# Performance work log

Measured on AMD Instinct MI355X. Metric: run time of the kernel, lower is better.

## Reference

```python
import jax, jax.numpy as jnp
import numpy as np
import math

HEADS = 16
D = 1024
HEAD_DIM = D // HEADS
SEQ = 2048
BATCH = 4
LN_EPS = 1e-5


def setup_inputs() -> dict:
    key = jax.random.key(0)
    ks = jax.random.split(key, 7)
    s = 1.0 / math.sqrt(HEAD_DIM)
    return {
        "q": jax.random.normal(ks[0], (SEQ, BATCH, D), dtype=jnp.float32),
        "k": jax.random.normal(ks[1], (SEQ, BATCH, D), dtype=jnp.float32),
        "v": jax.random.normal(ks[2], (SEQ, BATCH, D), dtype=jnp.float32),
        "Wq": jax.random.normal(ks[3], (HEAD_DIM, HEAD_DIM), dtype=jnp.float32) * s,
        "Wk": jax.random.normal(ks[4], (HEAD_DIM, HEAD_DIM), dtype=jnp.float32) * s,
        "Wv": jax.random.normal(ks[5], (HEAD_DIM, HEAD_DIM), dtype=jnp.float32) * s,
        "Wl": jax.random.normal(ks[6], (D, D), dtype=jnp.float32) * (1.0 / math.sqrt(D)),
        "gamma": jnp.ones((D,), dtype=jnp.float32),
        "beta": jnp.zeros((D,), dtype=jnp.float32),
    }


def reference(q, k, v, Wq, Wk, Wv, Wl, gamma, beta):
    # q, k, v: [seq_len, batch, d]  (seq-first, as in the torch module)
    q_len, batch = q.shape[0], q.shape[1]
    k_len, v_len = k.shape[0], v.shape[0]
    # Faithful to torch: reshape (NOT transpose) seq-first tensor into
    # (batch, len, heads, head_dim), then per-head linear (x @ W.T, no bias).
    Qh = jnp.einsum('bqhd,ed->bqhe', q.reshape(batch, q_len, HEADS, HEAD_DIM), Wq)
    Kh = jnp.einsum('bkhd,ed->bkhe', k.reshape(batch, k_len, HEADS, HEAD_DIM), Wk)
    Vh = jnp.einsum('bvhd,ed->bvhe', v.reshape(batch, v_len, HEADS, HEAD_DIM), Wv)
    # Scores scaled by sqrt(d) (full model dim), as in the original.
    scores = jnp.einsum('bqhd,bkhd->bhqk', Qh, Kh) / math.sqrt(D)
    attn = jax.nn.softmax(scores, axis=-1)  # dropout p=0.0 -> identity
    out = jnp.einsum('bhqk,bkhd->bqhd', attn, Vh)  # [b, q, h, d]
    concat = out.reshape(q_len, batch, D)
    lin = concat @ Wl.T
    mean = jnp.mean(lin, axis=-1, keepdims=True)
    var = jnp.var(lin, axis=-1, keepdims=True)
    ln = (lin - mean) * jax.lax.rsqrt(var + LN_EPS) * gamma + beta
    return q + ln
```

## Files before the change

kernel.cpp:

```cpp
#include <hip/hip_runtime.h>

#define LOG2E 1.4426950408889634f

typedef __attribute__((ext_vector_type(8))) short short8_t;
typedef __attribute__((ext_vector_type(4))) float floatx4;
typedef __attribute__((ext_vector_type(16))) float floatx16;

#define MFMA(a,b,c)   __builtin_amdgcn_mfma_f32_16x16x32_bf16(a,b,c,0,0,0)
#define MFMA32(a,b,c) __builtin_amdgcn_mfma_f32_32x32x16_bf16(a,b,c,0,0,0)
#define GLOAD(g, l) __builtin_amdgcn_global_load_lds( \
    (const __attribute__((address_space(1))) unsigned int*)(g), \
    (__attribute__((address_space(3))) unsigned int*)(l), 16, 0, 0)

__device__ __forceinline__ unsigned short f2bf(float f){
    unsigned u = __float_as_uint(f);
    u = u + 0x7FFFu + ((u >> 16) & 1u);
    return (unsigned short)(u >> 16);
}
__device__ __forceinline__ float bf2f(unsigned short s){
    return __uint_as_float(((unsigned)s) << 16);
}
__device__ __forceinline__ unsigned cvtpk(float lo, float hi){
    unsigned r;
    asm("v_cvt_pk_bf16_f32 %0, %1, %2" : "=v"(r) : "v"(lo), "v"(hi));
    return r;
}
__device__ __forceinline__ void plswap(unsigned &a, unsigned &b){
    asm volatile("v_permlane32_swap_b32 %0, %1" : "+v"(a), "+v"(b));
}

union U8 { unsigned u[4]; short8_t s8; };


__global__ __launch_bounds__(256) void proj_kernel(
    const float* __restrict__ Xq, const float* __restrict__ Xk, const float* __restrict__ Xv,
    const float* __restrict__ Wq, const float* __restrict__ Wk, const float* __restrict__ Wv,
    unsigned short* __restrict__ qp, unsigned short* __restrict__ kp, unsigned short* __restrict__ vp)
{
    const int rt = blockIdx.x;
    const int h  = blockIdx.y;
    const int sel= blockIdx.z;
    const float* X = (sel==0)?Xq:(sel==1)?Xk:Xv;
    const float* W = (sel==0)?Wq:(sel==1)?Wk:Wv;
    unsigned short* O = (sel==0)?qp:(sel==1)?kp:vp;
    const float qs = (sel==0) ? ((1.0f/32.0f)*LOG2E) : 1.0f;

    const int t  = threadIdx.x;
    const int w  = t >> 6, l = t & 63;
    const int r5 = l & 31;
    const int hf = l >> 5;

    const int row0 = rt*128 + w*32;

    short8_t a[4];
    {
        const float* xb = X + (size_t)(row0 + r5)*1024 + h*64 + hf*8;
        #pragma unroll
        for (int kb=0; kb<4; kb++){
            float4 f0 = *reinterpret_cast<const float4*>(xb + kb*16);
            float4 f1 = *reinterpret_cast<const float4*>(xb + kb*16 + 4);
            U8 u;
            u.u[0] = cvtpk(f0.x, f0.y); u.u[1] = cvtpk(f0.z, f0.w);
            u.u[2] = cvtpk(f1.x, f1.y); u.u[3] = cvtpk(f1.z, f1.w);
            a[kb] = u.s8;
        }
    }
    short8_t b[2][4];
    #pragma unroll
    for (int nb=0; nb<2; nb++){
        const float* wb = W + (size_t)(nb*32 + r5)*64 + hf*8;
        #pragma unroll
        for (int kb=0; kb<4; kb++){
            float4 f0 = *reinterpret_cast<const float4*>(wb + kb*16);
            float4 f1 = *reinterpret_cast<const float4*>(wb + kb*16 + 4);
            U8 u;
            u.u[0] = cvtpk(f0.x, f0.y); u.u[1] = cvtpk(f0.z, f0.w);
            u.u[2] = cvtpk(f1.x, f1.y); u.u[3] = cvtpk(f1.z, f1.w);
            b[nb][kb] = u.s8;
        }
    }

    floatx16 acc[2] = {};
    #pragma unroll
    for (int nb=0; nb<2; nb++)
        #pragma unroll
        for (int kb=0; kb<4; kb++)
            acc[nb] = MFMA32(a[kb], b[nb][kb], acc[nb]);

    const int c   = rt >> 4;
    const size_t chbase = (size_t)(c*16 + h);

    #pragma unroll
    for (int nb=0; nb<2; nb++){
        const int e = nb*32 + r5;
        #pragma unroll
        for (int m=0; m<4; m++){
            unsigned p01 = cvtpk(acc[nb][4*m]*qs,   acc[nb][4*m+1]*qs);
            unsigned p23 = cvtpk(acc[nb][4*m+2]*qs, acc[nb][4*m+3]*qs);
            #pragma unroll
            for (int i=0; i<4; i++){
                unsigned short val = (unsigned short)
                    ((i==0)?p01 : (i==1)?(p01>>16) : (i==2)?p23 : (p23>>16));
                const int gr = row0 + i + 8*m + 4*hf;
                const int s  = gr & 2047;
                size_t addr;
                if (sel == 0){
                    addr = (chbase*2048 + s)*64 + e;
                } else {
                    const int kt_ = s >> 6, rl = s & 63;
                    const size_t tbase = (chbase*32 + kt_)*4096;
                    if (sel == 1)
                        addr = tbase + rl*64 + (((e>>3) ^ (rl&7))<<3) + (e&7);
                    else
                        addr = tbase + e*64 + (((rl>>3) ^ (e&7))<<3) + (rl&7);
                }
                O[addr] = val;
            }
        }
    }
}

__global__ __launch_bounds__(256,1) void attn_kernel(
    const unsigned short* __restrict__ qp, const unsigned short* __restrict__ kp,
    const unsigned short* __restrict__ vp, unsigned short* __restrict__ ob)
{
    const int bswz = blockIdx.x;
    const int xr   = bswz & 7;
    const int rest = bswz >> 3;
    const int qt   = rest & 15;
    const int p    = xr + 8*(rest >> 4);
    const int hd   = p & 15;
    const int c    = p >> 4;

    const int t  = threadIdx.x;
    const int w  = t >> 6, l = t & 63;
    const int r5 = l & 31;
    const int hf = l >> 5;

    __shared__ unsigned short Ks[2][64][64];
    __shared__ unsigned short Vs[3][64][64];

    const size_t chq = ((size_t)(c*16 + hd))*2048*64;
    const size_t cht = ((size_t)(c*16 + hd))*32*4096;

    short8_t aq[4];
    {
        const unsigned short* qrow = qp + chq + (size_t)(qt*128 + w*32 + r5)*64 + hf*8;
        #pragma unroll
        for (int kb=0;kb<4;kb++)
            aq[kb] = *reinterpret_cast<const short8_t*>(qrow + kb*16);
    }

    const char* kbase = (const char*)(kp + cht) + w*2048 + l*16;
    const char* vbase = (const char*)(vp + cht) + w*2048 + l*16;
    char* kdst0 = (char*)(&Ks[0][0][0]) + w*2048;
    char* vdst0 = (char*)(&Vs[0][0][0]) + w*2048;

    #define ATTN_STAGE(kbuf, vbuf, kt) do { \
        const char* ks_ = kbase + (size_t)(kt)*8192; \
        const char* vs_ = vbase + (size_t)(kt)*8192; \
        char* kd_ = kdst0 + (kbuf)*8192; \
        char* vd_ = vdst0 + (vbuf)*8192; \
        GLOAD(ks_,      kd_);      GLOAD(ks_+1024, kd_+1024); \
        GLOAD(vs_,      vd_);      GLOAD(vs_+1024, vd_+1024); \
    } while(0)

    const int x7 = r5 & 7;

    U8 onesu;
    onesu.u[0] = 0x3F803F80u; onesu.u[1] = 0x3F803F80u;
    onesu.u[2] = 0x3F803F80u; onesu.u[3] = 0x3F803F80u;
    const short8_t ones8 = onesu.s8;

    floatx16 oa[2] = {};
    floatx16 lsv = {};
    short8_t Fp[4];

    ATTN_STAGE(0, 0, 0);

    int vcur = 0;
    for (int kt=0; kt<32; kt++){
        const int kcur = kt & 1;
        const int vnxt = (vcur==2) ? 0 : vcur+1;
        const int vprv = (vcur==0) ? 2 : vcur-1;

        asm volatile("s_waitcnt vmcnt(0)" ::: "memory");
        __builtin_amdgcn_s_barrier();
        __builtin_amdgcn_sched_barrier(0);

        if (kt < 31) ATTN_STAGE(kcur^1, vnxt, kt+1);

        const unsigned short* Kc = &Ks[kcur][0][0];
        const unsigned short* Vp = &Vs[vprv][0][0];

        floatx16 sacc[2] = {};
        __builtin_amdgcn_s_setprio(1);
        #pragma unroll
        for (int mb=0;mb<2;mb++){
            #pragma unroll
            for (int kb=0;kb<4;kb++){
                short8_t kf = *reinterpret_cast<const short8_t*>(
                    Kc + (mb*32 + r5)*64 + (((kb*2 + hf) ^ x7)<<3));
                sacc[mb] = MFMA32(kf, aq[kb], sacc[mb]);
            }
        }
        if (kt > 0){
            #pragma unroll
            for (int db=0;db<2;db++){
                #pragma unroll
                for (int kb2=0;kb2<4;kb2++){
                    short8_t vf = *reinterpret_cast<const short8_t*>(
                        Vp + (db*32 + r5)*64 + (((kb2*2 + hf) ^ x7)<<3));
                    oa[db] = MFMA32(vf, Fp[kb2], oa[db]);
                }
            }
            #pragma unroll
            for (int f=0;f<4;f++) lsv = MFMA32(ones8, Fp[f], lsv);
        }
        __builtin_amdgcn_s_setprio(0);

        #pragma unroll
        for (int mb=0;mb<2;mb++)
            #pragma unroll
            for (int i=0;i<16;i++)
                sacc[mb][i] = __builtin_amdgcn_exp2f(sacc[mb][i]);

        #pragma unroll
        for (int mb=0;mb<2;mb++){
            unsigned lo[4], hi[4];
            #pragma unroll
            for (int m=0;m<4;m++){
                lo[m] = cvtpk(sacc[mb][4*m],   sacc[mb][4*m+1]);
                hi[m] = cvtpk(sacc[mb][4*m+2], sacc[mb][4*m+3]);
            }
            #pragma unroll
            for (int hk=0;hk<2;hk++){
                unsigned a = lo[2*hk], b = lo[2*hk+1];
                unsigned cc = hi[2*hk], d = hi[2*hk+1];
                plswap(a, b);
                plswap(cc, d);
                U8 fu;
                fu.u[0] = a; fu.u[1] = cc; fu.u[2] = b; fu.u[3] = d;
                Fp[mb*2 + hk] = fu.s8;
            }
        }

        vcur = vnxt;
    }

    {
        const int vprv = (vcur==0) ? 2 : vcur-1;
        const unsigned short* Vp = &Vs[vprv][0][0];
        #pragma unroll
        for (int db=0;db<2;db++){
            #pragma unroll
            for (int kb2=0;kb2<4;kb2++){
                short8_t vf = *reinterpret_cast<const short8_t*>(
                    Vp + (db*32 + r5)*64 + (((kb2*2 + hf) ^ x7)<<3));
                oa[db] = MFMA32(vf, Fp[kb2], oa[db]);
            }
        }
        #pragma unroll
        for (int f=0;f<4;f++) lsv = MFMA32(ones8, Fp[f], lsv);
    }

    const float inv = 1.0f / lsv[0];
    const int rl_ = w*32 + r5;
    unsigned short* obimg = ob + ((size_t)((c*16 + qt)*16 + hd))*8192 + rl_*64;
    const int x7o = rl_ & 7;
    #pragma unroll
    for (int db=0;db<2;db++){
        #pragma unroll
        for (int m=0;m<4;m++){
            ushort4 u;
            u.x = f2bf(oa[db][4*m]*inv);   u.y = f2bf(oa[db][4*m+1]*inv);
            u.z = f2bf(oa[db][4*m+2]*inv); u.w = f2bf(oa[db][4*m+3]*inv);
            *reinterpret_cast<ushort4*>(obimg + (((db*4+m) ^ x7o)<<3) + hf*4) = u;
        }
    }
}

__global__ __launch_bounds__(256) void wlconv_kernel(const float* __restrict__ W,
                                                     unsigned short* __restrict__ O)
{
    int i = (blockIdx.x*256 + threadIdx.x)*4;
    const int n = i >> 10, k = i & 1023;
    float4 f = *reinterpret_cast<const float4*>(W + i);
    ushort4 u;
    u.x = f2bf(f.x); u.y = f2bf(f.y); u.z = f2bf(f.z); u.w = f2bf(f.w);
    const int rl = n & 127, cl = k & 63;
    size_t off = ((size_t)((n>>7)*16 + (k>>6)))*8192 + rl*64
               + (((cl>>3) ^ (rl&7))<<3) + (cl&7);
    *reinterpret_cast<ushort4*>(O + off) = u;
}

__global__ __launch_bounds__(256) void gemm_kernel(
    const unsigned short* __restrict__ A, const unsigned short* __restrict__ B,
    unsigned short* __restrict__ C)
{
    const int bm = blockIdx.x, bn = blockIdx.y;
    __shared__ unsigned short As[2][128][64];
    __shared__ unsigned short Bs[2][128][64];
    const int t = threadIdx.x, w = t>>6, l = t&63;
    const int l15 = l&15, l4 = l>>4;
    const int wm = w>>1, wn = w&1;
    const int x7g = l15 & 7;

    const char* abase = (const char*)A + (size_t)bm*16*16384 + w*4096 + l*16;
    const char* bbase = (const char*)B + (size_t)bn*16*16384 + w*4096 + l*16;
    char* adst = (char*)(&As[0][0][0]) + w*4096;
    char* bdst = (char*)(&Bs[0][0][0]) + w*4096;

    #define GEMM_STAGE(buf, kt) do { \
        const char* as_ = abase + (size_t)(kt)*16384; \
        const char* bs_ = bbase + (size_t)(kt)*16384; \
        char* ad_ = adst + (buf)*16384; \
        char* bd_ = bdst + (buf)*16384; \
        GLOAD(as_,       ad_);        GLOAD(as_+1024,  ad_+1024); \
        GLOAD(as_+2048,  ad_+2048);   GLOAD(as_+3072,  ad_+3072); \
        GLOAD(bs_,       bd_);        GLOAD(bs_+1024,  bd_+1024); \
        GLOAD(bs_+2048,  bd_+2048);   GLOAD(bs_+3072,  bd_+3072); \
    } while(0)

    floatx4 acc[4][4] = {};

    GEMM_STAGE(0, 0);

    for (int kt=0; kt<16; kt++){
        const int cur = kt & 1;
        if (kt < 15){
            GEMM_STAGE(cur^1, kt+1);
            asm volatile("s_waitcnt vmcnt(8)" ::: "memory");
        } else {
            asm volatile("s_waitcnt vmcnt(0)" ::: "memory");
        }
        __builtin_amdgcn_s_barrier();
        __builtin_amdgcn_sched_barrier(0);

        #pragma unroll
        for (int kk=0;kk<2;kk++){
            short8_t a[4], b[4];
            #pragma unroll
            for (int mt=0;mt<4;mt++){
                int row = wm*64 + mt*16 + l15;
                a[mt] = *reinterpret_cast<const short8_t*>(
                    &As[cur][0][0] + row*64 + (((kk*4 + l4) ^ x7g)<<3));
            }
            #pragma unroll
            for (int nt=0;nt<4;nt++){
                int row = wn*64 + nt*16 + l15;
                b[nt] = *reinterpret_cast<const short8_t*>(
                    &Bs[cur][0][0] + row*64 + (((kk*4 + l4) ^ x7g)<<3));
            }
            __builtin_amdgcn_s_setprio(1);
            #pragma unroll
            for (int mt=0;mt<4;mt++)
                #pragma unroll
                for (int nt=0;nt<4;nt++)
                    acc[mt][nt] = MFMA(a[mt], b[nt], acc[mt][nt]);
            __builtin_amdgcn_s_setprio(0);
        }

        __builtin_amdgcn_sched_barrier(0);
        __builtin_amdgcn_s_barrier();
    }

    #pragma unroll
    for (int mt=0;mt<4;mt++)
        #pragma unroll
        for (int nt=0;nt<4;nt++)
            #pragma unroll
            for (int j=0;j<4;j++){
                int row = bm*128 + wm*64 + mt*16 + l4*4 + j;
                int col = bn*128 + wn*64 + nt*16 + l15;
                C[(size_t)row*1024 + col] = f2bf(acc[mt][nt][j]);
            }
}

__global__ __launch_bounds__(256) void ln_kernel(
    const unsigned short* __restrict__ lin, const float* __restrict__ qin,
    const float* __restrict__ gamma, const float* __restrict__ beta, float* __restrict__ out)
{
    const int r = blockIdx.x, t = threadIdx.x;
    const unsigned short* row = lin + (size_t)r*1024;
    uint2 u = *reinterpret_cast<const uint2*>(row + t*4);
    float v0 = bf2f((unsigned short)(u.x & 0xffffu));
    float v1 = bf2f((unsigned short)(u.x >> 16));
    float v2 = bf2f((unsigned short)(u.y & 0xffffu));
    float v3 = bf2f((unsigned short)(u.y >> 16));
    float s  = v0+v1+v2+v3;
    float sq = v0*v0+v1*v1+v2*v2+v3*v3;
    #pragma unroll
    for (int d=1; d<64; d<<=1){ s += __shfl_xor(s, d); sq += __shfl_xor(sq, d); }
    __shared__ float red[8];
    if ((t&63)==0){ red[(t>>6)*2] = s; red[(t>>6)*2+1] = sq; }
    __syncthreads();
    s  = red[0]+red[2]+red[4]+red[6];
    sq = red[1]+red[3]+red[5]+red[7];
    float mean = s*(1.f/1024.f);
    float var  = sq*(1.f/1024.f) - mean*mean;
    float rs   = rsqrtf(var + 1e-5f);
    int base = r*1024 + t*4;
    float4 qv = *reinterpret_cast<const float4*>(qin + base);
    float4 g  = *reinterpret_cast<const float4*>(gamma + t*4);
    float4 b  = *reinterpret_cast<const float4*>(beta + t*4);
    float4 o;
    o.x = qv.x + (v0-mean)*rs*g.x + b.x;
    o.y = qv.y + (v1-mean)*rs*g.y + b.y;
    o.z = qv.z + (v2-mean)*rs*g.z + b.z;
    o.w = qv.w + (v3-mean)*rs*g.w + b.w;
    *reinterpret_cast<float4*>(out + base) = o;
}

extern "C" void kernel_launch(void* const* d_in, const int* in_sizes, int n_in,
                              void* d_out, int out_size, void* d_ws, size_t ws_size,
                              hipStream_t stream)
{
    (void)in_sizes; (void)n_in; (void)out_size; (void)ws_size;
    const float* q     = (const float*)d_in[0];
    const float* k     = (const float*)d_in[1];
    const float* v     = (const float*)d_in[2];
    const float* Wq    = (const float*)d_in[3];
    const float* Wk    = (const float*)d_in[4];
    const float* Wv    = (const float*)d_in[5];
    const float* Wl    = (const float*)d_in[6];
    const float* gamma = (const float*)d_in[7];
    const float* beta  = (const float*)d_in[8];
    float* out = (float*)d_out;

    char* ws = (char*)d_ws;
    unsigned short* qp  = (unsigned short*)(ws);
    unsigned short* kp  = (unsigned short*)(ws + (16u<<20));
    unsigned short* vp  = (unsigned short*)(ws + (32u<<20));
    unsigned short* ob  = (unsigned short*)(ws + (48u<<20));
    unsigned short* lin = (unsigned short*)(ws);
    unsigned short* wlb = (unsigned short*)(ws + (16u<<20));

    proj_kernel <<<dim3(64,16,3),  256, 0, stream>>>(q,k,v, Wq,Wk,Wv, qp,kp,vp);
    attn_kernel <<<dim3(1024),     256, 0, stream>>>(qp,kp,vp, ob);
    wlconv_kernel<<<dim3(1024),    256, 0, stream>>>(Wl, wlb);
    gemm_kernel <<<dim3(64,8),     256, 0, stream>>>(ob, wlb, lin);
    ln_kernel   <<<dim3(8192),     256, 0, stream>>>(lin, q, gamma, beta, out);
}
```

Measured before the change: 175.5 us.

## Fuse Q projection into attention kernel and swizzle GEMM block order

Removes the Q branch from the projection kernel. Each attention block now loads its fp32 Q rows, converts them to bf16 and runs the per-head Wq MFMA itself, then rearranges the accumulator into A-operand fragments with permlane32 swaps. This skips writing and re-reading the bf16 Q buffer. The first K/V stage is issued before this prologue so the loads overlap the projection. The GEMM also switches to a 1D grid with a grouped block mapping meant to improve L2 reuse of A and B tiles.

```diff
diff --git a/kernel.cpp b/kernel.cpp
--- a/kernel.cpp
+++ b/kernel.cpp
@@ -33,17 +33,16 @@
 
 
 __global__ __launch_bounds__(256) void proj_kernel(
-    const float* __restrict__ Xq, const float* __restrict__ Xk, const float* __restrict__ Xv,
-    const float* __restrict__ Wq, const float* __restrict__ Wk, const float* __restrict__ Wv,
-    unsigned short* __restrict__ qp, unsigned short* __restrict__ kp, unsigned short* __restrict__ vp)
+    const float* __restrict__ Xk, const float* __restrict__ Xv,
+    const float* __restrict__ Wk, const float* __restrict__ Wv,
+    unsigned short* __restrict__ kp, unsigned short* __restrict__ vp)
 {
     const int rt = blockIdx.x;
     const int h  = blockIdx.y;
     const int sel= blockIdx.z;
-    const float* X = (sel==0)?Xq:(sel==1)?Xk:Xv;
-    const float* W = (sel==0)?Wq:(sel==1)?Wk:Wv;
-    unsigned short* O = (sel==0)?qp:(sel==1)?kp:vp;
-    const float qs = (sel==0) ? ((1.0f/32.0f)*LOG2E) : 1.0f;
+    const float* X = sel ? Xv : Xk;
+    const float* W = sel ? Wv : Wk;
+    unsigned short* O = sel ? vp : kp;
 
     const int t  = threadIdx.x;
     const int w  = t >> 6, l = t & 63;
@@ -95,25 +94,21 @@
         const int e = nb*32 + r5;
         #pragma unroll
         for (int m=0; m<4; m++){
-            unsigned p01 = cvtpk(acc[nb][4*m]*qs,   acc[nb][4*m+1]*qs);
-            unsigned p23 = cvtpk(acc[nb][4*m+2]*qs, acc[nb][4*m+3]*qs);
+            unsigned p01 = cvtpk(acc[nb][4*m],   acc[nb][4*m+1]);
+            unsigned p23 = cvtpk(acc[nb][4*m+2], acc[nb][4*m+3]);
             #pragma unroll
             for (int i=0; i<4; i++){
                 unsigned short val = (unsigned short)
                     ((i==0)?p01 : (i==1)?(p01>>16) : (i==2)?p23 : (p23>>16));
                 const int gr = row0 + i + 8*m + 4*hf;
                 const int s  = gr & 2047;
+                const int kt_ = s >> 6, rl = s & 63;
+                const size_t tbase = (chbase*32 + kt_)*4096;
                 size_t addr;
-                if (sel == 0){
-                    addr = (chbase*2048 + s)*64 + e;
-                } else {
-                    const int kt_ = s >> 6, rl = s & 63;
-                    const size_t tbase = (chbase*32 + kt_)*4096;
-                    if (sel == 1)
-                        addr = tbase + rl*64 + (((e>>3) ^ (rl&7))<<3) + (e&7);
-                    else
-                        addr = tbase + e*64 + (((rl>>3) ^ (e&7))<<3) + (rl&7);
-                }
+                if (sel == 0)
+                    addr = tbase + rl*64 + (((e>>3) ^ (rl&7))<<3) + (e&7);
+                else
+                    addr = tbase + e*64 + (((rl>>3) ^ (e&7))<<3) + (rl&7);
                 O[addr] = val;
             }
         }
@@ -121,8 +116,9 @@
 }
 
 __global__ __launch_bounds__(256,1) void attn_kernel(
-    const unsigned short* __restrict__ qp, const unsigned short* __restrict__ kp,
-    const unsigned short* __restrict__ vp, unsigned short* __restrict__ ob)
+    const float* __restrict__ Xq, const float* __restrict__ Wq,
+    const unsigned short* __restrict__ kp, const unsigned short* __restrict__ vp,
+    unsigned short* __restrict__ ob)
 {
     const int bswz = blockIdx.x;
     const int xr   = bswz & 7;
@@ -140,16 +136,7 @@
     __shared__ unsigned short Ks[2][64][64];
     __shared__ unsigned short Vs[3][64][64];
 
-    const size_t chq = ((size_t)(c*16 + hd))*2048*64;
     const size_t cht = ((size_t)(c*16 + hd))*32*4096;
-
-    short8_t aq[4];
-    {
-        const unsigned short* qrow = qp + chq + (size_t)(qt*128 + w*32 + r5)*64 + hf*8;
-        #pragma unroll
-        for (int kb=0;kb<4;kb++)
-            aq[kb] = *reinterpret_cast<const short8_t*>(qrow + kb*16);
-    }
 
     const char* kbase = (const char*)(kp + cht) + w*2048 + l*16;
     const char* vbase = (const char*)(vp + cht) + w*2048 + l*16;
@@ -165,6 +152,57 @@
         GLOAD(vs_,      vd_);      GLOAD(vs_+1024, vd_+1024); \
     } while(0)
 
+    ATTN_STAGE(0, 0, 0);
+
+    short8_t aq[4];
+    {
+        short8_t bx[4];
+        const float* xb = Xq + (size_t)(c*2048 + qt*128 + w*32 + r5)*1024 + hd*64 + hf*8;
+        #pragma unroll
+        for (int kb=0; kb<4; kb++){
+            float4 f0 = *reinterpret_cast<const float4*>(xb + kb*16);
+            float4 f1 = *reinterpret_cast<const float4*>(xb + kb*16 + 4);
+            U8 u;
+            u.u[0] = cvtpk(f0.x, f0.y); u.u[1] = cvtpk(f0.z, f0.w);
+            u.u[2] = cvtpk(f1.x, f1.y); u.u[3] = cvtpk(f1.z, f1.w);
+            bx[kb] = u.s8;
+        }
+        floatx16 qa[2] = {};
+        #pragma unroll
+        for (int mb=0; mb<2; mb++){
+            const float* wb = Wq + (size_t)(mb*32 + r5)*64 + hf*8;
+            #pragma unroll
+            for (int kb=0; kb<4; kb++){
+                float4 f0 = *reinterpret_cast<const float4*>(wb + kb*16);
+                float4 f1 = *reinterpret_cast<const float4*>(wb + kb*16 + 4);
+                U8 u;
+                u.u[0] = cvtpk(f0.x, f0.y); u.u[1] = cvtpk(f0.z, f0.w);
+                u.u[2] = cvtpk(f1.x, f1.y); u.u[3] = cvtpk(f1.z, f1.w);
+                qa[mb] = MFMA32(u.s8, bx[kb], qa[mb]);
+            }
+        }
+        const float qs = (1.0f/32.0f)*LOG2E;
+        #pragma unroll
+        for (int mb=0; mb<2; mb++){
+            unsigned lo[4], hi[4];
+            #pragma unroll
+            for (int m=0;m<4;m++){
+                lo[m] = cvtpk(qa[mb][4*m]*qs,   qa[mb][4*m+1]*qs);
+                hi[m] = cvtpk(qa[mb][4*m+2]*qs, qa[mb][4*m+3]*qs);
+            }
+            #pragma unroll
+            for (int hk=0;hk<2;hk++){
+                unsigned a_ = lo[2*hk], b_ = lo[2*hk+1];
+                unsigned cc = hi[2*hk], d_ = hi[2*hk+1];
+                plswap(a_, b_);
+                plswap(cc, d_);
+                U8 fu;
+                fu.u[0] = a_; fu.u[1] = cc; fu.u[2] = b_; fu.u[3] = d_;
+                aq[mb*2 + hk] = fu.s8;
+            }
+        }
+    }
+
     const int x7 = r5 & 7;
 
     U8 onesu;
@@ -175,8 +213,6 @@
     floatx16 oa[2] = {};
     floatx16 lsv = {};
     short8_t Fp[4];
-
-    ATTN_STAGE(0, 0, 0);
 
     int vcur = 0;
     for (int kt=0; kt<32; kt++){
@@ -298,7 +334,11 @@
     const unsigned short* __restrict__ A, const unsigned short* __restrict__ B,
     unsigned short* __restrict__ C)
 {
-    const int bm = blockIdx.x, bn = blockIdx.y;
+    const int wg  = blockIdx.x;
+    const int xr  = wg & 7;
+    const int bn  = (wg >> 3) & 7;
+    const int bm  = ((wg >> 6) << 3) + xr;
+
     __shared__ unsigned short As[2][128][64];
     __shared__ unsigned short Bs[2][128][64];
     const int t = threadIdx.x, w = t>>6, l = t&63;
@@ -429,16 +469,15 @@
     float* out = (float*)d_out;
 
     char* ws = (char*)d_ws;
-    unsigned short* qp  = (unsigned short*)(ws);
     unsigned short* kp  = (unsigned short*)(ws + (16u<<20));
     unsigned short* vp  = (unsigned short*)(ws + (32u<<20));
     unsigned short* ob  = (unsigned short*)(ws + (48u<<20));
     unsigned short* lin = (unsigned short*)(ws);
     unsigned short* wlb = (unsigned short*)(ws + (16u<<20));
 
-    proj_kernel <<<dim3(64,16,3),  256, 0, stream>>>(q,k,v, Wq,Wk,Wv, qp,kp,vp);
-    attn_kernel <<<dim3(1024),     256, 0, stream>>>(qp,kp,vp, ob);
+    proj_kernel <<<dim3(64,16,2),  256, 0, stream>>>(k, v, Wk, Wv, kp, vp);
+    attn_kernel <<<dim3(1024),     256, 0, stream>>>(q, Wq, kp, vp, ob);
     wlconv_kernel<<<dim3(1024),    256, 0, stream>>>(Wl, wlb);
-    gemm_kernel <<<dim3(64,8),     256, 0, stream>>>(ob, wlb, lin);
+    gemm_kernel <<<dim3(512),      256, 0, stream>>>(ob, wlb, lin);
     ln_kernel   <<<dim3(8192),     256, 0, stream>>>(lin, q, gamma, beta, out);
 }
```

Measured after the change: 173.8 us. Within noise of the previous version (-1.0%).
